# Performance work log

Measured on AMD Instinct MI355X. Metric: run time of the kernel, lower is better.

## Reference

```python
import jax, jax.numpy as jnp
import numpy as np

N = 50000      # nodes
E = 800000     # edges
IN = 128       # in_dim
OUT = 64       # out_dim
NEG_SLOPE = 0.01  # F.leaky_relu default


def setup_inputs() -> dict:
    key = jax.random.key(0)
    k1, k2, k3, k4, k5 = jax.random.split(key, 5)
    h = jax.random.normal(k1, (N, IN), dtype=jnp.float32)
    # xavier-normal-ish scale for the two linear layers
    W_fc = jax.random.normal(k2, (OUT, IN), dtype=jnp.float32) * (2.0 / (IN + OUT)) ** 0.5
    W_attn = jax.random.normal(k3, (2 * OUT,), dtype=jnp.float32) * (2.0 / (2 * OUT + 1)) ** 0.5
    src = jax.random.randint(k4, (E,), 0, N)
    dst = jax.random.randint(k5, (E,), 0, N)
    return {"h": h, "W_fc": W_fc, "W_attn": W_attn, "src": src, "dst": dst}


def reference(h, W_fc, W_attn, src, dst):
    # z = fc(h): [N, OUT]
    z = jnp.einsum("ni,oi->no", h, W_fc)
    d = z.shape[-1]
    # per-edge attention logit: attn_fc(cat([z_src, z_dst])) == z_src@a_l + z_dst@a_r
    a_l, a_r = W_attn[:d], W_attn[d:]
    zs = z[src]                                   # [E, OUT] gather
    e = jax.nn.leaky_relu(zs @ a_l + z[dst] @ a_r, negative_slope=NEG_SLOPE)  # [E]
    # segment softmax over incoming edges of each dst node
    m = jax.ops.segment_max(e, dst, num_segments=N)          # [N]
    ex = jnp.exp(e - m[dst])                                  # [E]
    denom = jax.ops.segment_sum(ex, dst, num_segments=N)      # [N]
    alpha = ex / denom[dst]                                    # [E]
    # weighted scatter-sum of source features
    out = jax.ops.segment_sum(alpha[:, None] * zs, dst, num_segments=N)  # [N, OUT]
    return out
```

## Files before the change

kernel.cpp:

```cpp
#include <hip/hip_runtime.h>
#include <hip/hip_bf16.h>
#include <math.h>

#define IN_DIM 128
#define OUT_DIM 64
#define NEG_SLOPE 0.01f
#define BCAP 2048
#define EPT 16

typedef __attribute__((ext_vector_type(8))) short bf8_t;
typedef __attribute__((ext_vector_type(4))) float f4_t;

__device__ __forceinline__ bf8_t pack8(float4 a, float4 b) {
    union { bf8_t v; __hip_bfloat162 h[4]; } u;
    u.h[0] = __float22bfloat162_rn(make_float2(a.x, a.y));
    u.h[1] = __float22bfloat162_rn(make_float2(a.z, a.w));
    u.h[2] = __float22bfloat162_rn(make_float2(b.x, b.y));
    u.h[3] = __float22bfloat162_rn(make_float2(b.z, b.w));
    return u.v;
}

__global__ __launch_bounds__(256) void k_front(
    const int* __restrict__ src, const int* __restrict__ dst,
    int* __restrict__ bucket_cursor, unsigned* __restrict__ tmp, int E,
    const float4* __restrict__ h4, const float4* __restrict__ W4,
    const float* __restrict__ Wattn,
    __hip_bfloat16* __restrict__ zb, float* __restrict__ s_l, float* __restrict__ s_r,
    int N, int NP1)
{
    __shared__ int cnt[1024];
    __shared__ int cur[1024];

    if (blockIdx.x < NP1) {
        const int t = threadIdx.x;
        const int base_e = blockIdx.x * (256 * EPT);

        for (int b = t; b < 1024; b += 256) cnt[b] = 0;
        __syncthreads();

        unsigned pArr[EPT];
        #pragma unroll
        for (int i = 0; i < EPT; i++) {
            int ei = base_e + i * 256 + t;
            if (ei < E) {
                int s = src[ei], d = dst[ei];
                int b = d >> 6;
                pArr[i] = ((unsigned)b << 22) | ((unsigned)s << 6) | (unsigned)(d & 63);
                atomicAdd(&cnt[b], 1);
            } else {
                pArr[i] = 0xFFFFFFFFu;
            }
        }
        __syncthreads();

        for (int b = t; b < 1024; b += 256)
            if (cnt[b] > 0)
                cur[b] = atomicAdd(&bucket_cursor[b], cnt[b]);
        __syncthreads();

        #pragma unroll
        for (int i = 0; i < EPT; i++) {
            unsigned p = pArr[i];
            if (p == 0xFFFFFFFFu) continue;
            int b = p >> 22;
            int slot = atomicAdd(&cur[b], 1);
            if (slot < BCAP)
                tmp[(size_t)b * BCAP + slot] = p;
        }
    } else {
        const int lane = threadIdx.x & 63;
        const int wv   = threadIdx.x >> 6;
        const int col  = lane & 15, quad = lane >> 4;
        const int n0   = (blockIdx.x - NP1) * 64 + wv * 16;
        if (n0 >= N) return;

        bf8_t bf[4][4];
        #pragma unroll
        for (int ns = 0; ns < 4; ns++) {
            const float4* wrow = W4 + (size_t)(ns * 16 + col) * (IN_DIM / 4);
            #pragma unroll
            for (int kb = 0; kb < 4; kb++) {
                float4 x = wrow[kb * 8 + quad * 2];
                float4 y = wrow[kb * 8 + quad * 2 + 1];
                bf[kb][ns] = pack8(x, y);
            }
        }

        const int  na = n0 + col;
        const bool nv = (na < N);
        const float4* hrow = h4 + (size_t)(nv ? na : 0) * (IN_DIM / 4);
        const float4 zero = make_float4(0.f, 0.f, 0.f, 0.f);

        f4_t acc[4];
        #pragma unroll
        for (int ns = 0; ns < 4; ns++) acc[ns] = (f4_t){0.f, 0.f, 0.f, 0.f};

        #pragma unroll
        for (int kb = 0; kb < 4; kb++) {
            float4 x = nv ? hrow[kb * 8 + quad * 2]     : zero;
            float4 y = nv ? hrow[kb * 8 + quad * 2 + 1] : zero;
            bf8_t a = pack8(x, y);
            #pragma unroll
            for (int ns = 0; ns < 4; ns++)
                acc[ns] = __builtin_amdgcn_mfma_f32_16x16x32_bf16(a, bf[kb][ns], acc[ns], 0, 0, 0);
        }

        float alv[4], arv[4];
        #pragma unroll
        for (int ns = 0; ns < 4; ns++) {
            alv[ns] = Wattn[ns * 16 + col];
            arv[ns] = Wattn[OUT_DIM + ns * 16 + col];
        }
        #pragma unroll
        for (int r = 0; r < 4; r++) {
            const int nn = n0 + quad * 4 + r;
            float pl = acc[0][r] * alv[0] + acc[1][r] * alv[1] + acc[2][r] * alv[2] + acc[3][r] * alv[3];
            float pr = acc[0][r] * arv[0] + acc[1][r] * arv[1] + acc[2][r] * arv[2] + acc[3][r] * arv[3];
            #pragma unroll
            for (int o = 1; o < 16; o <<= 1) {
                pl += __shfl_xor(pl, o, 64);
                pr += __shfl_xor(pr, o, 64);
            }
            if (nn < N) {
                __hip_bfloat16* zr = zb + (size_t)nn * OUT_DIM;
                #pragma unroll
                for (int ns = 0; ns < 4; ns++)
                    zr[ns * 16 + col] = __float2bfloat16(acc[ns][r]);
                if (col == 0) { s_l[nn] = pl; s_r[nn] = pr; }
            }
        }
    }
}

__global__ __launch_bounds__(256) void k_tail(
    const unsigned* __restrict__ tmp, const int* __restrict__ bucket_cnt,
    const float* __restrict__ s_l, const float* __restrict__ s_r,
    const uint4* __restrict__ zb4, float4* __restrict__ out4, int N)
{
    __shared__ uint2 se[BCAP];
    __shared__ int cnt_s[64], off_s[64], cur_s[64];
    __shared__ float srs[64];

    const int b = blockIdx.x, t = threadIdx.x;
    const int lane = t & 63;
    const int nbase = b * 64;
    int mb = bucket_cnt[b];
    if (mb > BCAP) mb = BCAP;

    if (t < 64) {
        cnt_s[t] = 0;
        int n = nbase + t;
        srs[t] = (n < N) ? s_r[n] : 0.f;
    }
    __syncthreads();

    const unsigned* mybuf = tmp + (size_t)b * BCAP;

    for (int i = t; i < mb; i += 256)
        atomicAdd(&cnt_s[mybuf[i] & 63u], 1);
    __syncthreads();

    if (t < 64) {
        int c = cnt_s[t];
        int inc = c;
        #pragma unroll
        for (int o = 1; o < 64; o <<= 1) {
            int v = __shfl_up(inc, o, 64);
            if (lane >= o) inc += v;
        }
        off_s[t] = inc - c;
        cur_s[t] = inc - c;
    }
    __syncthreads();

    for (int i = t; i < mb; i += 256) {
        unsigned p = mybuf[i];
        int d = p & 63u;
        int s = (p >> 6) & 0xFFFFu;
        float e = s_l[s] + srs[d];
        e = (e > 0.f) ? e : NEG_SLOPE * e;
        float ex = __expf(e);
        int slot = atomicAdd(&cur_s[d], 1);
        se[slot] = make_uint2((unsigned)s, __float_as_uint(ex));
    }
    __syncthreads();

    const int ch8 = t & 7;
    const int grp = t >> 3;

    for (int nl = grp; nl < 64; nl += 32) {
        const int n = nbase + nl;
        if (n >= N) continue;
        const int beg = off_s[nl];
        const int end = beg + cnt_s[nl];
        float4* op = out4 + (size_t)n * 16 + ch8 * 2;

        if (end <= beg) {
            op[0] = make_float4(0.f, 0.f, 0.f, 0.f);
            op[1] = make_float4(0.f, 0.f, 0.f, 0.f);
            continue;
        }

        float a0 = 0.f, a1 = 0.f, a2 = 0.f, a3 = 0.f;
        float a4 = 0.f, a5 = 0.f, a6 = 0.f, a7 = 0.f;
        float dsum = 0.f;

        for (int i = beg; i < end; ++i) {
            uint2 q = se[i];
            float ex = __uint_as_float(q.y);
            dsum += ex;
            uint4 zv = zb4[(size_t)q.x * 8 + ch8];
            float f0 = __uint_as_float(zv.x << 16);
            float f1 = __uint_as_float(zv.x & 0xffff0000u);
            float f2 = __uint_as_float(zv.y << 16);
            float f3 = __uint_as_float(zv.y & 0xffff0000u);
            float f4 = __uint_as_float(zv.z << 16);
            float f5 = __uint_as_float(zv.z & 0xffff0000u);
            float f6 = __uint_as_float(zv.w << 16);
            float f7 = __uint_as_float(zv.w & 0xffff0000u);
            a0 += ex * f0; a1 += ex * f1; a2 += ex * f2; a3 += ex * f3;
            a4 += ex * f4; a5 += ex * f5; a6 += ex * f6; a7 += ex * f7;
        }

        float inv = 1.f / dsum;
        op[0] = make_float4(a0 * inv, a1 * inv, a2 * inv, a3 * inv);
        op[1] = make_float4(a4 * inv, a5 * inv, a6 * inv, a7 * inv);
    }
}

extern "C" void kernel_launch(void* const* d_in, const int* in_sizes, int n_in,
                              void* d_out, int out_size, void* d_ws, size_t ws_size,
                              hipStream_t stream)
{
    const float* h     = (const float*)d_in[0];
    const float* Wfc   = (const float*)d_in[1];
    const float* Wattn = (const float*)d_in[2];
    const int*   src   = (const int*)d_in[3];
    const int*   dst   = (const int*)d_in[4];
    const int N = in_sizes[0] / IN_DIM;
    const int E = in_sizes[3];
    const int NBK = (N + 63) / 64;
    const int NP1 = (E + 256 * EPT - 1) / (256 * EPT);

    __hip_bfloat16* zb = (__hip_bfloat16*)d_ws;
    float* s_l     = (float*)(zb + (size_t)N * OUT_DIM);
    float* s_r     = s_l + N;
    int*   bcursor = (int*)(s_r + N);
    unsigned* tmp  = (unsigned*)(bcursor + 1024);

    const int nblk_g = (N + 63) / 64;

    hipMemsetAsync(bcursor, 0, 1024 * sizeof(int), stream);

    k_front<<<NP1 + nblk_g, 256, 0, stream>>>(src, dst, bcursor, tmp, E,
                                              (const float4*)h, (const float4*)Wfc, Wattn,
                                              zb, s_l, s_r, N, NP1);
    k_tail <<<NBK, 256, 0, stream>>>(tmp, bcursor, s_l, s_r,
                                     (const uint4*)zb, (float4*)d_out, N);
}
```

Baseline: 140.6 us.

## Replace global-atomic bucketing with per-block fixed-slot bucket lists

```diff
diff --git a/kernel.cpp b/kernel.cpp
--- a/kernel.cpp
+++ b/kernel.cpp
@@ -5,8 +5,10 @@
 #define IN_DIM 128
 #define OUT_DIM 64
 #define NEG_SLOPE 0.01f
-#define BCAP 2048
-#define EPT 16
+#define NBUCK 1024
+#define P1E 8192
+#define CAP 48
+#define SECAP 1536
 
 typedef __attribute__((ext_vector_type(8))) short bf8_t;
 typedef __attribute__((ext_vector_type(4))) float f4_t;
@@ -21,57 +23,58 @@
 }
 
 __global__ __launch_bounds__(256) void k_front(
-    const int* __restrict__ src, const int* __restrict__ dst,
-    int* __restrict__ bucket_cursor, unsigned* __restrict__ tmp, int E,
+    const int* __restrict__ src, const int* __restrict__ dst, int E,
     const float4* __restrict__ h4, const float4* __restrict__ W4,
     const float* __restrict__ Wattn,
     __hip_bfloat16* __restrict__ zb, float* __restrict__ s_l, float* __restrict__ s_r,
+    unsigned* __restrict__ tmp,
+    int* __restrict__ cntg,
     int N, int NP1)
 {
-    __shared__ int cnt[1024];
-    __shared__ int cur[1024];
-
-    if (blockIdx.x < NP1) {
-        const int t = threadIdx.x;
-        const int base_e = blockIdx.x * (256 * EPT);
-
-        for (int b = t; b < 1024; b += 256) cnt[b] = 0;
+    __shared__ int cntA[NBUCK];
+    __shared__ int curA[NBUCK];
+
+    const int bid = blockIdx.x;
+    const int t = threadIdx.x;
+
+    if (bid < NP1) {
+        const int base_e = bid * P1E;
+        for (int i = t; i < NBUCK; i += 256) { cntA[i] = 0; curA[i] = 0; }
         __syncthreads();
 
-        unsigned pArr[EPT];
-        #pragma unroll
-        for (int i = 0; i < EPT; i++) {
+        unsigned pArr[32];
+        #pragma unroll
+        for (int i = 0; i < 32; i++) {
             int ei = base_e + i * 256 + t;
             if (ei < E) {
                 int s = src[ei], d = dst[ei];
-                int b = d >> 6;
-                pArr[i] = ((unsigned)b << 22) | ((unsigned)s << 6) | (unsigned)(d & 63);
-                atomicAdd(&cnt[b], 1);
+                pArr[i] = ((unsigned)(d >> 6) << 22) | ((unsigned)s << 6) | (unsigned)(d & 63);
+                atomicAdd(&cntA[d >> 6], 1);
             } else {
                 pArr[i] = 0xFFFFFFFFu;
             }
         }
         __syncthreads();
 
-        for (int b = t; b < 1024; b += 256)
-            if (cnt[b] > 0)
-                cur[b] = atomicAdd(&bucket_cursor[b], cnt[b]);
-        __syncthreads();
-
-        #pragma unroll
-        for (int i = 0; i < EPT; i++) {
+        for (int i = t; i < NBUCK; i += 256) {
+            int c = cntA[i];
+            cntg[(size_t)bid * NBUCK + i] = (c < CAP) ? c : CAP;
+        }
+
+        #pragma unroll
+        for (int i = 0; i < 32; i++) {
             unsigned p = pArr[i];
             if (p == 0xFFFFFFFFu) continue;
             int b = p >> 22;
-            int slot = atomicAdd(&cur[b], 1);
-            if (slot < BCAP)
-                tmp[(size_t)b * BCAP + slot] = p;
+            int slot = atomicAdd(&curA[b], 1);
+            if (slot < CAP)
+                tmp[((size_t)bid * NBUCK + b) * CAP + slot] = p & 0x3FFFFFu;
         }
     } else {
-        const int lane = threadIdx.x & 63;
-        const int wv   = threadIdx.x >> 6;
+        const int lane = t & 63;
+        const int wv   = t >> 6;
         const int col  = lane & 15, quad = lane >> 4;
-        const int n0   = (blockIdx.x - NP1) * 64 + wv * 16;
+        const int n0   = (bid - NP1) * 64 + wv * 16;
         if (n0 >= N) return;
 
         bf8_t bf[4][4];
@@ -133,19 +136,17 @@
 }
 
 __global__ __launch_bounds__(256) void k_tail(
-    const unsigned* __restrict__ tmp, const int* __restrict__ bucket_cnt,
+    const unsigned* __restrict__ tmp, const int* __restrict__ cntg,
     const float* __restrict__ s_l, const float* __restrict__ s_r,
-    const uint4* __restrict__ zb4, float4* __restrict__ out4, int N)
+    const uint4* __restrict__ zb4, float4* __restrict__ out4, int N, int NP1)
 {
-    __shared__ uint2 se[BCAP];
+    __shared__ uint2 se[SECAP];
     __shared__ int cnt_s[64], off_s[64], cur_s[64];
     __shared__ float srs[64];
 
     const int b = blockIdx.x, t = threadIdx.x;
     const int lane = t & 63;
     const int nbase = b * 64;
-    int mb = bucket_cnt[b];
-    if (mb > BCAP) mb = BCAP;
 
     if (t < 64) {
         cnt_s[t] = 0;
@@ -154,10 +155,14 @@
     }
     __syncthreads();
 
-    const unsigned* mybuf = tmp + (size_t)b * BCAP;
-
-    for (int i = t; i < mb; i += 256)
-        atomicAdd(&cnt_s[mybuf[i] & 63u], 1);
+    int myc = 0;
+    size_t fbase = 0;
+    if (t < NP1) {
+        myc = cntg[(size_t)t * NBUCK + b];
+        fbase = ((size_t)t * NBUCK + b) * CAP;
+        for (int i = 0; i < myc; i++)
+            atomicAdd(&cnt_s[tmp[fbase + i] & 63u], 1);
+    }
     __syncthreads();
 
     if (t < 64) {
@@ -173,15 +178,18 @@
     }
     __syncthreads();
 
-    for (int i = t; i < mb; i += 256) {
-        unsigned p = mybuf[i];
-        int d = p & 63u;
-        int s = (p >> 6) & 0xFFFFu;
-        float e = s_l[s] + srs[d];
-        e = (e > 0.f) ? e : NEG_SLOPE * e;
-        float ex = __expf(e);
-        int slot = atomicAdd(&cur_s[d], 1);
-        se[slot] = make_uint2((unsigned)s, __float_as_uint(ex));
+    if (t < NP1) {
+        for (int i = 0; i < myc; i++) {
+            unsigned p = tmp[fbase + i];
+            int d = p & 63u;
+            int s = (p >> 6) & 0xFFFFu;
+            float e = s_l[s] + srs[d];
+            e = (e > 0.f) ? e : NEG_SLOPE * e;
+            float ex = __expf(e);
+            int slot = atomicAdd(&cur_s[d], 1);
+            if (slot < SECAP)
+                se[slot] = make_uint2((unsigned)s, __float_as_uint(ex));
+        }
     }
     __syncthreads();
 
@@ -192,7 +200,8 @@
         const int n = nbase + nl;
         if (n >= N) continue;
         const int beg = off_s[nl];
-        const int end = beg + cnt_s[nl];
+        int end = beg + cnt_s[nl];
+        if (end > SECAP) end = SECAP;
         float4* op = out4 + (size_t)n * 16 + ch8 * 2;
 
         if (end <= beg) {
@@ -205,6 +214,7 @@
         float a4 = 0.f, a5 = 0.f, a6 = 0.f, a7 = 0.f;
         float dsum = 0.f;
 
+        #pragma unroll 2
         for (int i = beg; i < end; ++i) {
             uint2 q = se[i];
             float ex = __uint_as_float(q.y);
@@ -239,22 +249,18 @@
     const int*   dst   = (const int*)d_in[4];
     const int N = in_sizes[0] / IN_DIM;
     const int E = in_sizes[3];
-    const int NBK = (N + 63) / 64;
-    const int NP1 = (E + 256 * EPT - 1) / (256 * EPT);
+    const int NP1 = (E + P1E - 1) / P1E;
+    const int NG  = (N + 63) / 64;
 
     __hip_bfloat16* zb = (__hip_bfloat16*)d_ws;
-    float* s_l     = (float*)(zb + (size_t)N * OUT_DIM);
-    float* s_r     = s_l + N;
-    int*   bcursor = (int*)(s_r + N);
-    unsigned* tmp  = (unsigned*)(bcursor + 1024);
-
-    const int nblk_g = (N + 63) / 64;
-
-    hipMemsetAsync(bcursor, 0, 1024 * sizeof(int), stream);
-
-    k_front<<<NP1 + nblk_g, 256, 0, stream>>>(src, dst, bcursor, tmp, E,
-                                              (const float4*)h, (const float4*)Wfc, Wattn,
-                                              zb, s_l, s_r, N, NP1);
-    k_tail <<<NBK, 256, 0, stream>>>(tmp, bcursor, s_l, s_r,
-                                     (const uint4*)zb, (float4*)d_out, N);
-}
+    float* s_l    = (float*)(zb + (size_t)N * OUT_DIM);
+    float* s_r    = s_l + N;
+    int*   cntg   = (int*)(s_r + N);
+    unsigned* tmp = (unsigned*)(cntg + (size_t)NP1 * NBUCK);
+
+    k_front<<<NP1 + NG, 256, 0, stream>>>(src, dst, E,
+                                          (const float4*)h, (const float4*)Wfc, Wattn,
+                                          zb, s_l, s_r, tmp, cntg, N, NP1);
+    k_tail <<<NG, 256, 0, stream>>>(tmp, cntg, s_l, s_r,
+                                    (const uint4*)zb, (float4*)d_out, N, NP1);
+}
```

Measured after the change: 143.1 us. Within noise of the previous version (+1.8%).
